# Performance work log

Hardware: AMD Instinct MI355X
Metric: run time of the kernel (lower is better)

Reference implementation:

```python
import jax, jax.numpy as jnp
import numpy as np

N, E, G = 50000, 600000, 512   # nodes, edges, graphs
F, D, L = 128, 128, 3          # in_features, hidden dim, num_gc_layers
ED = D * L                      # embedding_dim (readout='concat')
C = 1.0                         # curvature
MIN_NORM = 1e-15
BALL_EPS = 4e-3                 # hgcn PoincareBall proj eps for float32


def _logmap0(p, c):
    sc = jnp.sqrt(c)
    n = jnp.clip(jnp.linalg.norm(p, axis=-1, keepdims=True), MIN_NORM, None)
    return p / (sc * n) * jnp.arctanh(jnp.clip(sc * n, -1 + 1e-15, 1 - 1e-15))


def _expmap0(u, c):
    sc = jnp.sqrt(c)
    n = jnp.clip(jnp.linalg.norm(u, axis=-1, keepdims=True), MIN_NORM, None)
    return jnp.tanh(sc * n) * u / (sc * n)


def _proj(x, c):
    n = jnp.clip(jnp.linalg.norm(x, axis=-1, keepdims=True), MIN_NORM, None)
    maxn = (1.0 - BALL_EPS) / jnp.sqrt(c)
    return jnp.where(n > maxn, x / n * maxn, x)


def _gcn(x, W, b, src, dst):
    h = x @ W
    deg = jax.ops.segment_sum(jnp.ones_like(dst, dtype=h.dtype), dst, num_segments=N) + 1.0
    dinv = deg ** -0.5
    msg = h[src] * (dinv[src] * dinv[dst])[:, None]           # [E, D]
    agg = jax.ops.segment_sum(msg, dst, num_segments=N) + h * (dinv * dinv)[:, None]
    return agg + b


def _encoder(x, Ws, bs, src, dst, batch):
    xs = []
    for W, b in zip(Ws, bs):
        x = jax.nn.relu(_gcn(x, W, b, src, dst))
        xs.append(x)
    # readout='concat' with global_add_pool
    g = jnp.concatenate([jax.ops.segment_sum(h, batch, num_segments=G) for h in xs], axis=1)
    return g, jnp.concatenate(xs, axis=1)


def _mlp(x, W1, W2):  # proj_head: Linear (no bias), ReLU, Linear (no bias)
    return jax.nn.relu(x @ W1) @ W2


def setup_inputs() -> dict:
    key = jax.random.key(0)
    ks = jax.random.split(key, 24)

    def xav(k, i, o):
        return jax.random.normal(k, (i, o), dtype=jnp.float32) * np.float32(np.sqrt(2.0 / (i + o)))

    inp = {
        'x':   jax.random.normal(ks[0], (N, F), dtype=jnp.float32) * 1e-3,  # points inside the ball
        'x_s': jax.random.normal(ks[1], (N, F), dtype=jnp.float32) * 1e-3,
        'src': jax.random.randint(ks[2], (E,), 0, N, dtype=jnp.int32),
        'dst': jax.random.randint(ks[3], (E,), 0, N, dtype=jnp.int32),
        'batch': jnp.sort(jax.random.randint(ks[4], (N,), 0, G, dtype=jnp.int32)),
        # feature-branch GCN encoder
        'Wf0': xav(ks[5], F, D), 'Wf1': xav(ks[6], D, D), 'Wf2': xav(ks[7], D, D),
        'bf0': jnp.zeros((D,), jnp.float32), 'bf1': jnp.zeros((D,), jnp.float32), 'bf2': jnp.zeros((D,), jnp.float32),
        # structure-branch GCN encoder
        'Ws0': xav(ks[8], F, D), 'Ws1': xav(ks[9], D, D), 'Ws2': xav(ks[10], D, D),
        'bs0': jnp.zeros((D,), jnp.float32), 'bs1': jnp.zeros((D,), jnp.float32), 'bs2': jnp.zeros((D,), jnp.float32),
        # proj heads (biases removed by init_emb)
        'P1': xav(ks[11], ED, ED), 'P2': xav(ks[12], ED, ED),
        'G1': xav(ks[13], 2 * ED, ED), 'G2': xav(ks[14], ED, ED),
    }
    return inp


def reference(x, x_s, Wf0, Wf1, Wf2, bf0, bf1, bf2, Ws0, Ws1, Ws2, bs0, bs1, bs2, P1, P2, G1, G2, src, dst, batch):
    xt_f = _logmap0(x, C)
    xt_s = _logmap0(x_s, C)
    g_f, n_f = _encoder(xt_f, (Wf0, Wf1, Wf2), (bf0, bf1, bf2), src, dst, batch)
    g_s, n_s = _encoder(xt_s, (Ws0, Ws1, Ws2), (bs0, bs1, bs2), src, dst, batch)
    g = _mlp(jnp.concatenate((g_f, g_s), axis=1), G1, G2)
    e = lambda t: _proj(_expmap0(t, C), C)
    return (e(g), e(_mlp(g_f, P1, P2)), e(_mlp(n_f, P1, P2)), e(_mlp(g_s, P1, P2)), e(_mlp(n_s, P1, P2)))
```

## Files before the change

### kernel.cpp

```cpp
#include <hip/hip_runtime.h>
#include <math.h>

#define N_NODES 50000
#define N_EDGES 600000
#define N_GRAPHS 512
#define F_IN 128
#define D_HID 128
#define EDIM 384
#define M_ALL (N_NODES + N_GRAPHS)

typedef __attribute__((ext_vector_type(8))) short bf16x8;
typedef __attribute__((ext_vector_type(4))) float f32x4;

static __device__ __forceinline__ float wave_reduce_sum(float s) {
#pragma unroll
  for (int off = 32; off > 0; off >>= 1) s += __shfl_xor(s, off, 64);
  return s;
}

static __device__ __forceinline__ int wave_reduce_sum_i(int s) {
#pragma unroll
  for (int off = 32; off > 0; off >>= 1) s += __shfl_xor(s, off, 64);
  return s;
}

static __device__ __forceinline__ short f2b(float f) {
  unsigned u = __float_as_uint(f);
  unsigned r = (u + 0x7FFFu + ((u >> 16) & 1u)) >> 16;
  return (short)r;
}

static __device__ __forceinline__ float b2f(short s) {
  return __uint_as_float(((unsigned)(unsigned short)s) << 16);
}


#define SCAN_BS 256
#define SCAN_NB ((N_NODES + SCAN_BS - 1) / SCAN_BS)

__global__ __launch_bounds__(SCAN_BS) void init_kernel(const int* __restrict__ batch,
                                                       int* __restrict__ cnt,
                                                       int* __restrict__ gptr) {
  int i = blockIdx.x * SCAN_BS + threadIdx.x;
  if (i < N_NODES) cnt[i] = 0;
  if (i <= N_GRAPHS) {
    int lo = 0, hi = N_NODES;
    while (lo < hi) { int mid = (lo + hi) >> 1; if (batch[mid] < i) lo = mid + 1; else hi = mid; }
    gptr[i] = lo;
  }
}

__global__ void hist_kernel(const int* __restrict__ dst, int* __restrict__ cnt) {
  int i = blockIdx.x * blockDim.x + threadIdx.x;
  if (i < N_EDGES) atomicAdd(&cnt[dst[i]], 1);
}

__global__ __launch_bounds__(SCAN_BS) void scan1_kernel(const int* __restrict__ cnt,
                                                        int* __restrict__ row_ptr,
                                                        int* __restrict__ bsum) {
  __shared__ int wsum[4];
  int tid = threadIdx.x, lane = tid & 63, wid = tid >> 6;
  int idx = blockIdx.x * SCAN_BS + tid;
  int v = (idx < N_NODES) ? cnt[idx] : 0;
  int x = v;
#pragma unroll
  for (int off = 1; off < 64; off <<= 1) {
    int t = __shfl_up(x, off, 64);
    if (lane >= off) x += t;
  }
  if (lane == 63) wsum[wid] = x;
  __syncthreads();
  int pre = 0, tot = 0;
#pragma unroll
  for (int w = 0; w < 4; ++w) { int s = wsum[w]; tot += s; if (w < wid) pre += s; }
  if (idx < N_NODES) row_ptr[idx + 1] = x + pre;
  if (tid == 0) bsum[blockIdx.x] = tot;
}

__global__ __launch_bounds__(SCAN_BS) void scan3_kernel(const int* __restrict__ cnt,
                                                        const int* __restrict__ bsum,
                                                        int* __restrict__ row_ptr,
                                                        int* __restrict__ cursor,
                                                        float* __restrict__ dinv) {
  __shared__ int ws[4];
  int tid = threadIdx.x, lane = tid & 63, wid = tid >> 6;
  int v = 0;
  if (tid < SCAN_NB && tid < blockIdx.x) v = bsum[tid];
  v = wave_reduce_sum_i(v);
  if (lane == 0) ws[wid] = v;
  __syncthreads();
  int boff = ws[0] + ws[1] + ws[2] + ws[3];
  int idx = blockIdx.x * SCAN_BS + tid;
  if (idx >= N_NODES) return;
  int val = row_ptr[idx + 1] + boff;
  row_ptr[idx + 1] = val;
  int c = cnt[idx];
  cursor[idx] = val - c;
  dinv[idx] = 1.0f / sqrtf((float)(c + 1));
  if (idx == 0) row_ptr[0] = 0;
}

__global__ void scatter_kernel(const int* __restrict__ src, const int* __restrict__ dst,
                               const float* __restrict__ dinv, int* __restrict__ cursor,
                               int* __restrict__ col, float* __restrict__ ew) {
  int e = blockIdx.x * blockDim.x + threadIdx.x;
  if (e >= N_EDGES) return;
  int s = src[e], d = dst[e];
  int pos = atomicAdd(&cursor[d], 1);
  col[pos] = s;
  ew[pos] = dinv[s] * dinv[d];
}


struct WcSeg { const float* W; short* Wt; int K; int Nc; };
struct WcArgs { WcSeg seg[10]; };

__global__ void wconv_all_kernel(WcArgs a) {
  int sidx = blockIdx.y;
  WcSeg s = a.seg[sidx];
  int i = blockIdx.x * blockDim.x + threadIdx.x;
  if (i >= s.K * s.Nc) return;
  int k = i / s.Nc, n = i - k * s.Nc;
  s.Wt[(size_t)n * s.K + k] = f2b(s.W[i]);
}


__global__ __launch_bounds__(256) void logmap2_kernel(const float* __restrict__ x,
                                                      const float* __restrict__ x_s,
                                                      short* __restrict__ Ab) {
  int w = blockIdx.x * 4 + (threadIdx.x >> 6);
  int lane = threadIdx.x & 63;
  if (w >= 2 * N_NODES) return;
  int br = (w >= N_NODES) ? 1 : 0;
  int row = br ? (w - N_NODES) : w;
  const float* xr = (br ? x_s : x) + (size_t)row * F_IN;
  float2 v = *(const float2*)(xr + lane * 2);
  float s = wave_reduce_sum(v.x * v.x + v.y * v.y);
  float n = sqrtf(s);
  float nc = fmaxf(n, 1e-15f);
  float f = atanhf(fminf(nc, 0.9999999f)) / nc;
  short2 o; o.x = f2b(v.x * f); o.y = f2b(v.y * f);
  *(short2*)(Ab + (size_t)row * 256 + br * 128 + lane * 2) = o;
}


__global__ __launch_bounds__(256) void agg2_kernel(const short* __restrict__ Xin, int lda,
                                                   const float* __restrict__ dinv,
                                                   const int* __restrict__ row_ptr,
                                                   const int* __restrict__ col,
                                                   const float* __restrict__ ew,
                                                   short* __restrict__ Xa) {
  int node = blockIdx.x * 4 + (threadIdx.x >> 6);
  int lane = threadIdx.x & 63;
  if (node >= N_NODES) return;
  float di = dinv[node];
  float wsf = di * di;
  short4 sv = *(const short4*)(Xin + (size_t)node * lda + lane * 4);
  float a0 = b2f(sv.x) * wsf, a1 = b2f(sv.y) * wsf, a2 = b2f(sv.z) * wsf, a3 = b2f(sv.w) * wsf;
  int s = row_ptr[node], e = row_ptr[node + 1];
  int j = s;
  for (; j + 4 <= e; j += 4) {
    int c0 = col[j], c1 = col[j + 1], c2 = col[j + 2], c3 = col[j + 3];
    float w0 = ew[j], w1 = ew[j + 1], w2 = ew[j + 2], w3 = ew[j + 3];
    short4 v0 = *(const short4*)(Xin + (size_t)c0 * lda + lane * 4);
    short4 v1 = *(const short4*)(Xin + (size_t)c1 * lda + lane * 4);
    short4 v2 = *(const short4*)(Xin + (size_t)c2 * lda + lane * 4);
    short4 v3 = *(const short4*)(Xin + (size_t)c3 * lda + lane * 4);
    a0 += b2f(v0.x) * w0; a1 += b2f(v0.y) * w0; a2 += b2f(v0.z) * w0; a3 += b2f(v0.w) * w0;
    a0 += b2f(v1.x) * w1; a1 += b2f(v1.y) * w1; a2 += b2f(v1.z) * w1; a3 += b2f(v1.w) * w1;
    a0 += b2f(v2.x) * w2; a1 += b2f(v2.y) * w2; a2 += b2f(v2.z) * w2; a3 += b2f(v2.w) * w2;
    a0 += b2f(v3.x) * w3; a1 += b2f(v3.y) * w3; a2 += b2f(v3.z) * w3; a3 += b2f(v3.w) * w3;
  }
  for (; j < e; ++j) {
    float w0 = ew[j];
    short4 v0 = *(const short4*)(Xin + (size_t)col[j] * lda + lane * 4);
    a0 += b2f(v0.x) * w0; a1 += b2f(v0.y) * w0; a2 += b2f(v0.z) * w0; a3 += b2f(v0.w) * w0;
  }
  short4 o; o.x = f2b(a0); o.y = f2b(a1); o.z = f2b(a2); o.w = f2b(a3);
  *(short4*)(Xa + (size_t)node * 256 + lane * 4) = o;
}


#define LDK 40

struct GemmZArgs {
  const short* A[2];
  const short* Bt[2];
  const float* bias[2];
  short* Cb[2];
  int lda, ldc, M, Nc, K, kexp, do_relu;
};

__global__ __launch_bounds__(256) void mfma_gemmz_kernel(GemmZArgs g) {
  __shared__ __align__(16) short As[128 * LDK];
  __shared__ __align__(16) short Bs[128 * LDK];
  int z = blockIdx.z;
  const short* __restrict__ A = g.A[z];
  const short* __restrict__ Bt = g.Bt[z];
  int tid = threadIdx.x;
  int wave = tid >> 6, lane = tid & 63;
  int wr = (wave >> 1) * 64, wc = (wave & 1) * 64;
  int q = lane >> 4, m = lane & 15;
  int row0 = blockIdx.x * 128, col0 = blockIdx.y * 128;
  f32x4 acc[4][4] = {};
  for (int k0 = 0; k0 < g.K; k0 += 32) {
#pragma unroll
    for (int p = 0; p < 2; ++p) {
      int idx = p * 256 + tid;
      int r = idx >> 2, kc = (idx & 3) * 8;
      int gr = row0 + r;
      int kk = k0 + kc;
      int acol = g.kexp ? (kk + ((kk >> 7) << 7)) : kk;
      float4 v = make_float4(0.f, 0.f, 0.f, 0.f);
      if (gr < g.M) v = *(const float4*)(A + (size_t)gr * g.lda + acol);
      *(float4*)(As + r * LDK + kc) = v;
      float4 w = *(const float4*)(Bt + (size_t)(col0 + r) * g.K + kk);
      *(float4*)(Bs + r * LDK + kc) = w;
    }
    __syncthreads();
    bf16x8 af[4], bfr[4];
#pragma unroll
    for (int i = 0; i < 4; ++i) {
      af[i]  = *(const bf16x8*)(As + (wr + i * 16 + m) * LDK + q * 8);
      bfr[i] = *(const bf16x8*)(Bs + (wc + i * 16 + m) * LDK + q * 8);
    }
#pragma unroll
    for (int i = 0; i < 4; ++i)
#pragma unroll
      for (int j = 0; j < 4; ++j)
        acc[i][j] = __builtin_amdgcn_mfma_f32_16x16x32_bf16(af[i], bfr[j], acc[i][j], 0, 0, 0);
    __syncthreads();
  }
  const float* __restrict__ bias = g.bias[z];
  short* __restrict__ Cb = g.Cb[z];
#pragma unroll
  for (int i = 0; i < 4; ++i) {
#pragma unroll
    for (int r = 0; r < 4; ++r) {
      int rr = row0 + wr + i * 16 + q * 4 + r;
      if (rr >= g.M) continue;
#pragma unroll
      for (int j = 0; j < 4; ++j) {
        int cc = col0 + wc + j * 16 + m;
        float v = acc[i][j][r];
        if (bias) v += bias[cc];
        if (g.do_relu) v = fmaxf(v, 0.0f);
        Cb[(size_t)rr * g.ldc + cc] = f2b(v);
      }
    }
  }
}


struct Head2Args {
  const short* A[2];
  const short* Bt2;
  float* Cf[2];
  float* Cf2[2];
  int lda, M, split;
};

__global__ __launch_bounds__(512) void head2_kernel(Head2Args g) {
  __shared__ __align__(16) short As[128 * LDK];
  __shared__ __align__(16) short Bs[384 * LDK];
  int z = blockIdx.z;
  const short* __restrict__ A = g.A[z];
  const short* __restrict__ Bt = g.Bt2;
  int tid = threadIdx.x;
  int wave = tid >> 6, lane = tid & 63;
  int q = lane >> 4, m = lane & 15;
  int row0 = blockIdx.x * 128;
  f32x4 acc[24] = {};
  for (int k0 = 0; k0 < 384; k0 += 32) {
    {
      int r = tid >> 2, kc = (tid & 3) * 8;
      int gr = row0 + r;
      float4 v = make_float4(0.f, 0.f, 0.f, 0.f);
      if (gr < g.M) v = *(const float4*)(A + (size_t)gr * g.lda + k0 + kc);
      *(float4*)(As + r * LDK + kc) = v;
    }
#pragma unroll
    for (int p = 0; p < 3; ++p) {
      int idx = p * 512 + tid;
      int r = idx >> 2, kc = (idx & 3) * 8;
      float4 w0 = *(const float4*)(Bt + (size_t)r * 384 + k0 + kc);
      *(float4*)(Bs + r * LDK + kc) = w0;
    }
    __syncthreads();
    bf16x8 af = *(const bf16x8*)(As + (wave * 16 + m) * LDK + q * 8);
#pragma unroll
    for (int j = 0; j < 24; ++j) {
      bf16x8 bfr = *(const bf16x8*)(Bs + (j * 16 + m) * LDK + q * 8);
      acc[j] = __builtin_amdgcn_mfma_f32_16x16x32_bf16(af, bfr, acc[j], 0, 0, 0);
    }
    __syncthreads();
  }
  float* __restrict__ Cf = g.Cf[z];
  float* __restrict__ Cf2 = g.Cf2[z];
  const float maxn = 1.0f - 4e-3f;
#pragma unroll
  for (int r = 0; r < 4; ++r) {
    float s = 0.0f;
#pragma unroll
    for (int j = 0; j < 24; ++j) s += acc[j][r] * acc[j][r];
    s += __shfl_xor(s, 1, 64);
    s += __shfl_xor(s, 2, 64);
    s += __shfl_xor(s, 4, 64);
    s += __shfl_xor(s, 8, 64);
    int rr = row0 + wave * 16 + q * 4 + r;
    if (rr >= g.M) continue;
    float n = fmaxf(sqrtf(s), 1e-15f);
    float th = tanhf(n);
    float f = th / n;
    float n2 = fmaxf(th, 1e-15f);
    if (n2 > maxn) f *= maxn / n2;
    if (rr < g.split) {
#pragma unroll
      for (int j = 0; j < 24; ++j) Cf[(size_t)rr * 384 + j * 16 + m] = acc[j][r] * f;
    } else {
#pragma unroll
      for (int j = 0; j < 24; ++j) Cf2[(size_t)(rr - g.split) * 384 + j * 16 + m] = acc[j][r] * f;
    }
  }
}


__global__ __launch_bounds__(768) void pool2_kernel(const short* __restrict__ NB,
                                                    const int* __restrict__ gptr,
                                                    short* __restrict__ GCb,
                                                    short* __restrict__ nbappend) {
  int g = blockIdx.x, t = threadIdx.x;
  int s = gptr[g], e = gptr[g + 1];
  float acc = 0.0f;
  for (int i = s; i < e; ++i) acc += b2f(NB[(size_t)i * 768 + t]);
  short bv = f2b(acc);
  int l = t >> 8, rem = t & 255, b = rem >> 7, c = rem & 127;
  GCb[(size_t)g * 768 + b * 384 + l * 128 + c] = bv;
  nbappend[(size_t)g * 768 + t] = bv;
}


extern "C" void kernel_launch(void* const* d_in, const int* in_sizes, int n_in,
                              void* d_out, int out_size, void* d_ws, size_t ws_size,
                              hipStream_t stream) {
  (void)in_sizes; (void)n_in; (void)out_size; (void)ws_size;
  const float* x   = (const float*)d_in[0];
  const float* x_s = (const float*)d_in[1];
  const int* src   = (const int*)d_in[2];
  const int* dst   = (const int*)d_in[3];
  const int* batch = (const int*)d_in[4];
  const float* Wf[3] = {(const float*)d_in[5], (const float*)d_in[6], (const float*)d_in[7]};
  const float* bf[3] = {(const float*)d_in[8], (const float*)d_in[9], (const float*)d_in[10]};
  const float* Wsb[3] = {(const float*)d_in[11], (const float*)d_in[12], (const float*)d_in[13]};
  const float* bs[3] = {(const float*)d_in[14], (const float*)d_in[15], (const float*)d_in[16]};
  const float* P1 = (const float*)d_in[17];
  const float* P2 = (const float*)d_in[18];
  const float* G1 = (const float*)d_in[19];
  const float* G2 = (const float*)d_in[20];
  float* out = (float*)d_out;

  char* w = (char*)d_ws;
  auto alloc = [&](size_t bytes) {
    char* p = w;
    w += (bytes + 255) & ~(size_t)255;
    return p;
  };
  short* HIDb2 = (short*)alloc((size_t)2 * M_ALL * 384 * 2);
  short* Ab    = HIDb2;
  short* Xa    = (short*)alloc((size_t)N_NODES * 256 * 2);
  short* NB    = (short*)alloc((size_t)M_ALL * 768 * 2);
  int* cnt     = (int*)alloc((size_t)N_NODES * 4);
  int* row_ptr = (int*)alloc((size_t)(N_NODES + 1) * 4);
  int* cursor  = (int*)alloc((size_t)N_NODES * 4);
  float* dinv  = (float*)alloc((size_t)N_NODES * 4);
  int* col     = (int*)alloc((size_t)N_EDGES * 4);
  float* ew    = (float*)alloc((size_t)N_EDGES * 4);
  int* gptr    = (int*)alloc((size_t)(N_GRAPHS + 1) * 4);
  int* bsum    = (int*)alloc(256 * 4);
  short* GCb   = (short*)alloc((size_t)N_GRAPHS * 768 * 2);
  short* GHb   = (short*)alloc((size_t)N_GRAPHS * 384 * 2);
  short* P1t   = (short*)alloc((size_t)EDIM * EDIM * 2);
  short* P2t   = (short*)alloc((size_t)EDIM * EDIM * 2);
  short* G1t   = (short*)alloc((size_t)768 * EDIM * 2);
  short* G2t   = (short*)alloc((size_t)EDIM * EDIM * 2);
  short* Wft[3], *Wst[3];
  for (int l = 0; l < 3; ++l) {
    Wft[l] = (short*)alloc((size_t)128 * 128 * 2);
    Wst[l] = (short*)alloc((size_t)128 * 128 * 2);
  }

  {
    WcArgs wa;
    wa.seg[0] = {P1, P1t, EDIM, EDIM};
    wa.seg[1] = {P2, P2t, EDIM, EDIM};
    wa.seg[2] = {G1, G1t, 768, EDIM};
    wa.seg[3] = {G2, G2t, EDIM, EDIM};
    for (int l = 0; l < 3; ++l) {
      wa.seg[4 + l] = {Wf[l], Wft[l], 128, 128};
      wa.seg[7 + l] = {Wsb[l], Wst[l], 128, 128};
    }
    wconv_all_kernel<<<dim3((768 * EDIM + 255) / 256, 10), 256, 0, stream>>>(wa);
  }

  init_kernel<<<SCAN_NB, SCAN_BS, 0, stream>>>(batch, cnt, gptr);
  hist_kernel<<<(N_EDGES + 255) / 256, 256, 0, stream>>>(dst, cnt);
  scan1_kernel<<<SCAN_NB, SCAN_BS, 0, stream>>>(cnt, row_ptr, bsum);
  scan3_kernel<<<SCAN_NB, SCAN_BS, 0, stream>>>(cnt, bsum, row_ptr, cursor, dinv);
  scatter_kernel<<<(N_EDGES + 255) / 256, 256, 0, stream>>>(src, dst, dinv, cursor, col, ew);

  const size_t OUT0 = 0;
  const size_t OUT1 = (size_t)N_GRAPHS * EDIM;
  const size_t OUT2 = OUT1 + (size_t)N_GRAPHS * EDIM;
  const size_t OUT3 = OUT2 + (size_t)N_NODES * EDIM;

  const int gx_layer = (N_NODES + 127) / 128;
  const int gx_mfma  = (M_ALL + 127) / 128;
  const int gx_agg   = (N_NODES + 3) / 4;

  logmap2_kernel<<<(2 * N_NODES + 3) / 4, 256, 0, stream>>>(x, x_s, Ab);

  const short* cur = Ab;
  int clda = 256;
  for (int l = 0; l < 3; ++l) {
    agg2_kernel<<<gx_agg, 256, 0, stream>>>(cur, clda, dinv, row_ptr, col, ew, Xa);
    GemmZArgs ga = {};
    ga.A[0] = Xa;        ga.A[1] = Xa + 128;
    ga.Bt[0] = Wft[l];   ga.Bt[1] = Wst[l];
    ga.bias[0] = bf[l];  ga.bias[1] = bs[l];
    ga.Cb[0] = NB + l * 256;        ga.Cb[1] = NB + l * 256 + 128;
    ga.lda = 256; ga.ldc = 768; ga.M = N_NODES; ga.Nc = 128; ga.K = 128;
    ga.kexp = 0; ga.do_relu = 1;
    mfma_gemmz_kernel<<<dim3(gx_layer, 1, 2), 256, 0, stream>>>(ga);
    cur = NB + l * 256;
    clda = 768;
  }

  pool2_kernel<<<N_GRAPHS, 768, 0, stream>>>(NB, gptr, GCb, NB + (size_t)N_NODES * 768);

  const int gx_g = (N_GRAPHS + 127) / 128;
  {
    GemmZArgs g1 = {};
    g1.A[0] = g1.A[1] = GCb;
    g1.Bt[0] = g1.Bt[1] = G1t;
    g1.Cb[0] = g1.Cb[1] = GHb;
    g1.lda = 768; g1.ldc = 384; g1.M = N_GRAPHS; g1.Nc = EDIM; g1.K = 768;
    g1.kexp = 0; g1.do_relu = 1;
    mfma_gemmz_kernel<<<dim3(gx_g, 3, 1), 256, 0, stream>>>(g1);

    Head2Args g2 = {};
    g2.A[0] = g2.A[1] = GHb;
    g2.Bt2 = G2t;
    g2.Cf[0] = g2.Cf[1] = out + OUT0;
    g2.Cf2[0] = g2.Cf2[1] = out + OUT0;
    g2.lda = 384; g2.M = N_GRAPHS; g2.split = 1 << 30;
    head2_kernel<<<dim3(gx_g, 1, 1), 512, 0, stream>>>(g2);
  }

  float* ghead_out[2] = {out + OUT1, out + OUT3};
  float* node_out[2]  = {out + OUT2, out + OUT3 + (size_t)N_GRAPHS * EDIM};
  {
    GemmZArgs h1 = {};
    h1.A[0] = NB;                 h1.A[1] = NB + 128;
    h1.Bt[0] = h1.Bt[1] = P1t;
    h1.Cb[0] = HIDb2;             h1.Cb[1] = HIDb2 + (size_t)M_ALL * 384;
    h1.lda = 768; h1.ldc = 384; h1.M = M_ALL; h1.Nc = EDIM; h1.K = EDIM;
    h1.kexp = 1; h1.do_relu = 1;
    mfma_gemmz_kernel<<<dim3(gx_mfma, 3, 2), 256, 0, stream>>>(h1);

    Head2Args h2 = {};
    h2.A[0] = HIDb2;              h2.A[1] = HIDb2 + (size_t)M_ALL * 384;
    h2.Bt2 = P2t;
    h2.Cf[0] = node_out[0];       h2.Cf[1] = node_out[1];
    h2.Cf2[0] = ghead_out[0];     h2.Cf2[1] = ghead_out[1];
    h2.lda = 384; h2.M = M_ALL; h2.split = N_NODES;
    head2_kernel<<<dim3(gx_mfma, 1, 2), 512, 0, stream>>>(h2);
  }
}
```

Baseline: 770.5 us.

## Fuse both projection-head MLP layers into one kernel keeping hidden in LDS

```diff
diff --git a/kernel.cpp b/kernel.cpp
--- a/kernel.cpp
+++ b/kernel.cpp
@@ -252,74 +252,130 @@
 }
 
 
-struct Head2Args {
+#define HLD 392
+
+struct Mlp2Args {
   const short* A[2];
-  const short* Bt2;
+  const short* B1;
+  const short* B2;
   float* Cf[2];
   float* Cf2[2];
-  int lda, M, split;
+  int lda, M, K1, kexp, split;
 };
 
-__global__ __launch_bounds__(512) void head2_kernel(Head2Args g) {
+__global__ __launch_bounds__(512, 2) void mlp2_kernel(Mlp2Args g) {
   __shared__ __align__(16) short As[128 * LDK];
   __shared__ __align__(16) short Bs[384 * LDK];
+  __shared__ __align__(16) short H[128 * HLD];
+  __shared__ float nsum[128][2];
   int z = blockIdx.z;
   const short* __restrict__ A = g.A[z];
-  const short* __restrict__ Bt = g.Bt2;
   int tid = threadIdx.x;
   int wave = tid >> 6, lane = tid & 63;
   int q = lane >> 4, m = lane & 15;
+  int rbase = (wave & 3) * 32;
+  int cg = wave >> 2;
   int row0 = blockIdx.x * 128;
-  f32x4 acc[24] = {};
-  for (int k0 = 0; k0 < 384; k0 += 32) {
+  f32x4 acc[2][12] = {};
+  for (int k0 = 0; k0 < g.K1; k0 += 32) {
     {
       int r = tid >> 2, kc = (tid & 3) * 8;
       int gr = row0 + r;
+      int kk = k0 + kc;
+      int acol = g.kexp ? (kk + ((kk >> 7) << 7)) : kk;
       float4 v = make_float4(0.f, 0.f, 0.f, 0.f);
-      if (gr < g.M) v = *(const float4*)(A + (size_t)gr * g.lda + k0 + kc);
+      if (gr < g.M) v = *(const float4*)(A + (size_t)gr * g.lda + acol);
       *(float4*)(As + r * LDK + kc) = v;
     }
 #pragma unroll
     for (int p = 0; p < 3; ++p) {
       int idx = p * 512 + tid;
       int r = idx >> 2, kc = (idx & 3) * 8;
-      float4 w0 = *(const float4*)(Bt + (size_t)r * 384 + k0 + kc);
+      float4 w0 = *(const float4*)(g.B1 + (size_t)r * g.K1 + k0 + kc);
       *(float4*)(Bs + r * LDK + kc) = w0;
     }
     __syncthreads();
-    bf16x8 af = *(const bf16x8*)(As + (wave * 16 + m) * LDK + q * 8);
-#pragma unroll
-    for (int j = 0; j < 24; ++j) {
-      bf16x8 bfr = *(const bf16x8*)(Bs + (j * 16 + m) * LDK + q * 8);
-      acc[j] = __builtin_amdgcn_mfma_f32_16x16x32_bf16(af, bfr, acc[j], 0, 0, 0);
+    bf16x8 af0 = *(const bf16x8*)(As + (rbase + m) * LDK + q * 8);
+    bf16x8 af1 = *(const bf16x8*)(As + (rbase + 16 + m) * LDK + q * 8);
+#pragma unroll
+    for (int j = 0; j < 12; ++j) {
+      bf16x8 bfr = *(const bf16x8*)(Bs + (cg * 192 + j * 16 + m) * LDK + q * 8);
+      acc[0][j] = __builtin_amdgcn_mfma_f32_16x16x32_bf16(af0, bfr, acc[0][j], 0, 0, 0);
+      acc[1][j] = __builtin_amdgcn_mfma_f32_16x16x32_bf16(af1, bfr, acc[1][j], 0, 0, 0);
     }
     __syncthreads();
   }
+#pragma unroll
+  for (int sub = 0; sub < 2; ++sub)
+#pragma unroll
+    for (int j = 0; j < 12; ++j)
+#pragma unroll
+      for (int r = 0; r < 4; ++r)
+        H[(rbase + sub * 16 + q * 4 + r) * HLD + cg * 192 + j * 16 + m] =
+            f2b(fmaxf(acc[sub][j][r], 0.0f));
+#pragma unroll
+  for (int sub = 0; sub < 2; ++sub)
+#pragma unroll
+    for (int j = 0; j < 12; ++j) acc[sub][j] = (f32x4){0.f, 0.f, 0.f, 0.f};
+  for (int k0 = 0; k0 < 384; k0 += 32) {
+#pragma unroll
+    for (int p = 0; p < 3; ++p) {
+      int idx = p * 512 + tid;
+      int r = idx >> 2, kc = (idx & 3) * 8;
+      float4 w0 = *(const float4*)(g.B2 + (size_t)r * 384 + k0 + kc);
+      *(float4*)(Bs + r * LDK + kc) = w0;
+    }
+    __syncthreads();
+    bf16x8 af0 = *(const bf16x8*)(H + (rbase + m) * HLD + k0 + q * 8);
+    bf16x8 af1 = *(const bf16x8*)(H + (rbase + 16 + m) * HLD + k0 + q * 8);
+#pragma unroll
+    for (int j = 0; j < 12; ++j) {
+      bf16x8 bfr = *(const bf16x8*)(Bs + (cg * 192 + j * 16 + m) * LDK + q * 8);
+      acc[0][j] = __builtin_amdgcn_mfma_f32_16x16x32_bf16(af0, bfr, acc[0][j], 0, 0, 0);
+      acc[1][j] = __builtin_amdgcn_mfma_f32_16x16x32_bf16(af1, bfr, acc[1][j], 0, 0, 0);
+    }
+    __syncthreads();
+  }
+#pragma unroll
+  for (int sub = 0; sub < 2; ++sub) {
+#pragma unroll
+    for (int r = 0; r < 4; ++r) {
+      float s = 0.0f;
+#pragma unroll
+      for (int j = 0; j < 12; ++j) s += acc[sub][j][r] * acc[sub][j][r];
+      s += __shfl_xor(s, 1, 64);
+      s += __shfl_xor(s, 2, 64);
+      s += __shfl_xor(s, 4, 64);
+      s += __shfl_xor(s, 8, 64);
+      if (m == 0) nsum[rbase + sub * 16 + q * 4 + r][cg] = s;
+    }
+  }
+  __syncthreads();
+  const float maxn = 1.0f - 4e-3f;
   float* __restrict__ Cf = g.Cf[z];
   float* __restrict__ Cf2 = g.Cf2[z];
-  const float maxn = 1.0f - 4e-3f;
-#pragma unroll
-  for (int r = 0; r < 4; ++r) {
-    float s = 0.0f;
-#pragma unroll
-    for (int j = 0; j < 24; ++j) s += acc[j][r] * acc[j][r];
-    s += __shfl_xor(s, 1, 64);
-    s += __shfl_xor(s, 2, 64);
-    s += __shfl_xor(s, 4, 64);
-    s += __shfl_xor(s, 8, 64);
-    int rr = row0 + wave * 16 + q * 4 + r;
-    if (rr >= g.M) continue;
-    float n = fmaxf(sqrtf(s), 1e-15f);
-    float th = tanhf(n);
-    float f = th / n;
-    float n2 = fmaxf(th, 1e-15f);
-    if (n2 > maxn) f *= maxn / n2;
-    if (rr < g.split) {
-#pragma unroll
-      for (int j = 0; j < 24; ++j) Cf[(size_t)rr * 384 + j * 16 + m] = acc[j][r] * f;
-    } else {
-#pragma unroll
-      for (int j = 0; j < 24; ++j) Cf2[(size_t)(rr - g.split) * 384 + j * 16 + m] = acc[j][r] * f;
+#pragma unroll
+  for (int sub = 0; sub < 2; ++sub) {
+#pragma unroll
+    for (int r = 0; r < 4; ++r) {
+      int rl = rbase + sub * 16 + q * 4 + r;
+      int rr = row0 + rl;
+      if (rr >= g.M) continue;
+      float s = nsum[rl][0] + nsum[rl][1];
+      float n = fmaxf(sqrtf(s), 1e-15f);
+      float th = tanhf(n);
+      float f = th / n;
+      float n2 = fmaxf(th, 1e-15f);
+      if (n2 > maxn) f *= maxn / n2;
+      if (rr < g.split) {
+#pragma unroll
+        for (int j = 0; j < 12; ++j)
+          Cf[(size_t)rr * 384 + cg * 192 + j * 16 + m] = acc[sub][j][r] * f;
+      } else {
+#pragma unroll
+        for (int j = 0; j < 12; ++j)
+          Cf2[(size_t)(rr - g.split) * 384 + cg * 192 + j * 16 + m] = acc[sub][j][r] * f;
+      }
     }
   }
 }
@@ -365,8 +421,7 @@
     w += (bytes + 255) & ~(size_t)255;
     return p;
   };
-  short* HIDb2 = (short*)alloc((size_t)2 * M_ALL * 384 * 2);
-  short* Ab    = HIDb2;
+  short* Ab    = (short*)alloc((size_t)N_NODES * 256 * 2);
   short* Xa    = (short*)alloc((size_t)N_NODES * 256 * 2);
   short* NB    = (short*)alloc((size_t)M_ALL * 768 * 2);
   int* cnt     = (int*)alloc((size_t)N_NODES * 4);
@@ -378,7 +433,6 @@
   int* gptr    = (int*)alloc((size_t)(N_GRAPHS + 1) * 4);
   int* bsum    = (int*)alloc(256 * 4);
   short* GCb   = (short*)alloc((size_t)N_GRAPHS * 768 * 2);
-  short* GHb   = (short*)alloc((size_t)N_GRAPHS * 384 * 2);
   short* P1t   = (short*)alloc((size_t)EDIM * EDIM * 2);
   short* P2t   = (short*)alloc((size_t)EDIM * EDIM * 2);
   short* G1t   = (short*)alloc((size_t)768 * EDIM * 2);
@@ -437,42 +491,23 @@
 
   pool2_kernel<<<N_GRAPHS, 768, 0, stream>>>(NB, gptr, GCb, NB + (size_t)N_NODES * 768);
 
-  const int gx_g = (N_GRAPHS + 127) / 128;
   {
-    GemmZArgs g1 = {};
-    g1.A[0] = g1.A[1] = GCb;
-    g1.Bt[0] = g1.Bt[1] = G1t;
-    g1.Cb[0] = g1.Cb[1] = GHb;
-    g1.lda = 768; g1.ldc = 384; g1.M = N_GRAPHS; g1.Nc = EDIM; g1.K = 768;
-    g1.kexp = 0; g1.do_relu = 1;
-    mfma_gemmz_kernel<<<dim3(gx_g, 3, 1), 256, 0, stream>>>(g1);
-
-    Head2Args g2 = {};
-    g2.A[0] = g2.A[1] = GHb;
-    g2.Bt2 = G2t;
-    g2.Cf[0] = g2.Cf[1] = out + OUT0;
-    g2.Cf2[0] = g2.Cf2[1] = out + OUT0;
-    g2.lda = 384; g2.M = N_GRAPHS; g2.split = 1 << 30;
-    head2_kernel<<<dim3(gx_g, 1, 1), 512, 0, stream>>>(g2);
-  }
-
-  float* ghead_out[2] = {out + OUT1, out + OUT3};
-  float* node_out[2]  = {out + OUT2, out + OUT3 + (size_t)N_GRAPHS * EDIM};
+    Mlp2Args gh = {};
+    gh.A[0] = gh.A[1] = GCb;
+    gh.B1 = G1t; gh.B2 = G2t;
+    gh.Cf[0] = gh.Cf[1] = out + OUT0;
+    gh.Cf2[0] = gh.Cf2[1] = out + OUT0;
+    gh.lda = 768; gh.M = N_GRAPHS; gh.K1 = 768; gh.kexp = 0; gh.split = 1 << 30;
+    mlp2_kernel<<<dim3((N_GRAPHS + 127) / 128, 1, 1), 512, 0, stream>>>(gh);
+  }
+
   {
-    GemmZArgs h1 = {};
-    h1.A[0] = NB;                 h1.A[1] = NB + 128;
-    h1.Bt[0] = h1.Bt[1] = P1t;
-    h1.Cb[0] = HIDb2;             h1.Cb[1] = HIDb2 + (size_t)M_ALL * 384;
-    h1.lda = 768; h1.ldc = 384; h1.M = M_ALL; h1.Nc = EDIM; h1.K = EDIM;
-    h1.kexp = 1; h1.do_relu = 1;
-    mfma_gemmz_kernel<<<dim3(gx_mfma, 3, 2), 256, 0, stream>>>(h1);
-
-    Head2Args h2 = {};
-    h2.A[0] = HIDb2;              h2.A[1] = HIDb2 + (size_t)M_ALL * 384;
-    h2.Bt2 = P2t;
-    h2.Cf[0] = node_out[0];       h2.Cf[1] = node_out[1];
-    h2.Cf2[0] = ghead_out[0];     h2.Cf2[1] = ghead_out[1];
-    h2.lda = 384; h2.M = M_ALL; h2.split = N_NODES;
-    head2_kernel<<<dim3(gx_mfma, 1, 2), 512, 0, stream>>>(h2);
-  }
-}
+    Mlp2Args h = {};
+    h.A[0] = NB;                  h.A[1] = NB + 128;
+    h.B1 = P1t; h.B2 = P2t;
+    h.Cf[0] = out + OUT2;         h.Cf[1] = out + OUT3 + (size_t)N_GRAPHS * EDIM;
+    h.Cf2[0] = out + OUT1;        h.Cf2[1] = out + OUT3;
+    h.lda = 768; h.M = M_ALL; h.K1 = EDIM; h.kexp = 1; h.split = N_NODES;
+    mlp2_kernel<<<dim3(gx_mfma, 1, 2), 512, 0, stream>>>(h);
+  }
+}
```

After: 766.6 us. About the same (-0.5%).

## Fuse two-layer projection MLPs into one kernel with hidden activations in LDS

Applied to the files above, without the earlier changes.

```diff
diff --git a/kernel.cpp b/kernel.cpp
--- a/kernel.cpp
+++ b/kernel.cpp
@@ -11,6 +11,7 @@
 
 typedef __attribute__((ext_vector_type(8))) short bf16x8;
 typedef __attribute__((ext_vector_type(4))) float f32x4;
+typedef __attribute__((ext_vector_type(16))) float f32x16;
 
 static __device__ __forceinline__ float wave_reduce_sum(float s) {
 #pragma unroll
@@ -252,76 +253,123 @@
 }
 
 
-struct Head2Args {
-  const short* A[2];
-  const short* Bt2;
-  float* Cf[2];
-  float* Cf2[2];
-  int lda, M, split;
+#define HLD 392
+
+struct MlpProb {
+  const short* A;
+  const short* B1;
+  const short* B2;
+  float* Cf;
+  float* Cf2;
+  int lda, M, K1, kexp, split;
 };
-
-__global__ __launch_bounds__(512) void head2_kernel(Head2Args g) {
-  __shared__ __align__(16) short As[128 * LDK];
-  __shared__ __align__(16) short Bs[384 * LDK];
+struct Mlp2Args { MlpProb p[3]; int gx_h; };
+
+__global__ __launch_bounds__(512) void mlp2_kernel(Mlp2Args g) {
+  __shared__ __align__(16) short H[128 * HLD];
+  __shared__ float nsum[128][4];
   int z = blockIdx.z;
-  const short* __restrict__ A = g.A[z];
-  const short* __restrict__ Bt = g.Bt2;
+  int bx = blockIdx.x;
+  MlpProb p;
+  int row0;
+  if (bx < g.gx_h) { p = g.p[z]; row0 = bx * 128; }
+  else { if (z) return; p = g.p[2]; row0 = (bx - g.gx_h) * 128; }
+
   int tid = threadIdx.x;
   int wave = tid >> 6, lane = tid & 63;
-  int q = lane >> 4, m = lane & 15;
-  int row0 = blockIdx.x * 128;
-  f32x4 acc[24] = {};
-  for (int k0 = 0; k0 < 384; k0 += 32) {
-    {
-      int r = tid >> 2, kc = (tid & 3) * 8;
-      int gr = row0 + r;
-      float4 v = make_float4(0.f, 0.f, 0.f, 0.f);
-      if (gr < g.M) v = *(const float4*)(A + (size_t)gr * g.lda + k0 + kc);
-      *(float4*)(As + r * LDK + kc) = v;
-    }
-#pragma unroll
-    for (int p = 0; p < 3; ++p) {
-      int idx = p * 512 + tid;
-      int r = idx >> 2, kc = (idx & 3) * 8;
-      float4 w0 = *(const float4*)(Bt + (size_t)r * 384 + k0 + kc);
-      *(float4*)(Bs + r * LDK + kc) = w0;
-    }
-    __syncthreads();
-    bf16x8 af = *(const bf16x8*)(As + (wave * 16 + m) * LDK + q * 8);
-#pragma unroll
-    for (int j = 0; j < 24; ++j) {
-      bf16x8 bfr = *(const bf16x8*)(Bs + (j * 16 + m) * LDK + q * 8);
-      acc[j] = __builtin_amdgcn_mfma_f32_16x16x32_bf16(af, bfr, acc[j], 0, 0, 0);
-    }
-    __syncthreads();
-  }
-  float* __restrict__ Cf = g.Cf[z];
-  float* __restrict__ Cf2 = g.Cf2[z];
+  int l31 = lane & 31, lh = lane >> 5;
+  int rg = wave & 1;
+  int cq = wave >> 1;
+
+  const short* Arow0 = p.A + (size_t)(row0 + rg * 64 + l31) * p.lda;
+  const short* Arow1 = Arow0 + (size_t)32 * p.lda;
+  const short* B1c0 = p.B1 + (size_t)(cq * 96 + l31) * p.K1;
+  const short* B1c1 = B1c0 + (size_t)32 * p.K1;
+  const short* B1c2 = B1c1 + (size_t)32 * p.K1;
+
+  f32x16 acc0[2][3] = {};
+#pragma unroll 2
+  for (int k0 = 0; k0 < p.K1; k0 += 16) {
+    int kk = k0 + lh * 8;
+    int acol = p.kexp ? (kk + ((kk >> 7) << 7)) : kk;
+    bf16x8 a0 = *(const bf16x8*)(Arow0 + acol);
+    bf16x8 a1 = *(const bf16x8*)(Arow1 + acol);
+    bf16x8 b0 = *(const bf16x8*)(B1c0 + kk);
+    bf16x8 b1 = *(const bf16x8*)(B1c1 + kk);
+    bf16x8 b2 = *(const bf16x8*)(B1c2 + kk);
+    acc0[0][0] = __builtin_amdgcn_mfma_f32_32x32x16_bf16(a0, b0, acc0[0][0], 0, 0, 0);
+    acc0[1][0] = __builtin_amdgcn_mfma_f32_32x32x16_bf16(a1, b0, acc0[1][0], 0, 0, 0);
+    acc0[0][1] = __builtin_amdgcn_mfma_f32_32x32x16_bf16(a0, b1, acc0[0][1], 0, 0, 0);
+    acc0[1][1] = __builtin_amdgcn_mfma_f32_32x32x16_bf16(a1, b1, acc0[1][1], 0, 0, 0);
+    acc0[0][2] = __builtin_amdgcn_mfma_f32_32x32x16_bf16(a0, b2, acc0[0][2], 0, 0, 0);
+    acc0[1][2] = __builtin_amdgcn_mfma_f32_32x32x16_bf16(a1, b2, acc0[1][2], 0, 0, 0);
+  }
+#pragma unroll
+  for (int rf = 0; rf < 2; ++rf)
+#pragma unroll
+    for (int f = 0; f < 3; ++f)
+#pragma unroll
+      for (int reg = 0; reg < 16; ++reg) {
+        int rl = rg * 64 + rf * 32 + (reg & 3) + 8 * (reg >> 2) + 4 * lh;
+        H[rl * HLD + cq * 96 + f * 32 + l31] = f2b(fmaxf(acc0[rf][f][reg], 0.0f));
+      }
+  __syncthreads();
+  const short* B2c0 = p.B2 + (size_t)(cq * 96 + l31) * 384;
+  const short* B2c1 = B2c0 + (size_t)32 * 384;
+  const short* B2c2 = B2c1 + (size_t)32 * 384;
+  const short* H0 = H + (rg * 64 + l31) * HLD;
+  const short* H1 = H0 + 32 * HLD;
+  f32x16 acc[2][3] = {};
+#pragma unroll 2
+  for (int k0 = 0; k0 < 384; k0 += 16) {
+    int kk = k0 + lh * 8;
+    bf16x8 a0 = *(const bf16x8*)(H0 + kk);
+    bf16x8 a1 = *(const bf16x8*)(H1 + kk);
+    bf16x8 b0 = *(const bf16x8*)(B2c0 + kk);
+    bf16x8 b1 = *(const bf16x8*)(B2c1 + kk);
+    bf16x8 b2 = *(const bf16x8*)(B2c2 + kk);
+    acc[0][0] = __builtin_amdgcn_mfma_f32_32x32x16_bf16(a0, b0, acc[0][0], 0, 0, 0);
+    acc[1][0] = __builtin_amdgcn_mfma_f32_32x32x16_bf16(a1, b0, acc[1][0], 0, 0, 0);
+    acc[0][1] = __builtin_amdgcn_mfma_f32_32x32x16_bf16(a0, b1, acc[0][1], 0, 0, 0);
+    acc[1][1] = __builtin_amdgcn_mfma_f32_32x32x16_bf16(a1, b1, acc[1][1], 0, 0, 0);
+    acc[0][2] = __builtin_amdgcn_mfma_f32_32x32x16_bf16(a0, b2, acc[0][2], 0, 0, 0);
+    acc[1][2] = __builtin_amdgcn_mfma_f32_32x32x16_bf16(a1, b2, acc[1][2], 0, 0, 0);
+  }
+#pragma unroll
+  for (int rf = 0; rf < 2; ++rf)
+#pragma unroll
+    for (int reg = 0; reg < 16; ++reg) {
+      float s = acc[rf][0][reg] * acc[rf][0][reg] + acc[rf][1][reg] * acc[rf][1][reg] +
+                acc[rf][2][reg] * acc[rf][2][reg];
+      s += __shfl_xor(s, 1, 64);
+      s += __shfl_xor(s, 2, 64);
+      s += __shfl_xor(s, 4, 64);
+      s += __shfl_xor(s, 8, 64);
+      s += __shfl_xor(s, 16, 64);
+      if (l31 == 0)
+        nsum[rg * 64 + rf * 32 + (reg & 3) + 8 * (reg >> 2) + 4 * lh][cq] = s;
+    }
+  __syncthreads();
   const float maxn = 1.0f - 4e-3f;
 #pragma unroll
-  for (int r = 0; r < 4; ++r) {
-    float s = 0.0f;
-#pragma unroll
-    for (int j = 0; j < 24; ++j) s += acc[j][r] * acc[j][r];
-    s += __shfl_xor(s, 1, 64);
-    s += __shfl_xor(s, 2, 64);
-    s += __shfl_xor(s, 4, 64);
-    s += __shfl_xor(s, 8, 64);
-    int rr = row0 + wave * 16 + q * 4 + r;
-    if (rr >= g.M) continue;
-    float n = fmaxf(sqrtf(s), 1e-15f);
-    float th = tanhf(n);
-    float f = th / n;
-    float n2 = fmaxf(th, 1e-15f);
-    if (n2 > maxn) f *= maxn / n2;
-    if (rr < g.split) {
-#pragma unroll
-      for (int j = 0; j < 24; ++j) Cf[(size_t)rr * 384 + j * 16 + m] = acc[j][r] * f;
-    } else {
-#pragma unroll
-      for (int j = 0; j < 24; ++j) Cf2[(size_t)(rr - g.split) * 384 + j * 16 + m] = acc[j][r] * f;
-    }
-  }
+  for (int rf = 0; rf < 2; ++rf)
+#pragma unroll
+    for (int reg = 0; reg < 16; ++reg) {
+      int rl = rg * 64 + rf * 32 + (reg & 3) + 8 * (reg >> 2) + 4 * lh;
+      int rr = row0 + rl;
+      if (rr >= p.M) continue;
+      float s = nsum[rl][0] + nsum[rl][1] + nsum[rl][2] + nsum[rl][3];
+      float n = fmaxf(sqrtf(s), 1e-15f);
+      float th = tanhf(n);
+      float fct = th / n;
+      float n2 = fmaxf(th, 1e-15f);
+      if (n2 > maxn) fct *= maxn / n2;
+      float* base = (rr < p.split) ? (p.Cf + (size_t)rr * 384)
+                                   : (p.Cf2 + (size_t)(rr - p.split) * 384);
+#pragma unroll
+      for (int f = 0; f < 3; ++f)
+        base[cq * 96 + f * 32 + l31] = acc[rf][f][reg] * fct;
+    }
 }
 
 
@@ -365,8 +413,7 @@
     w += (bytes + 255) & ~(size_t)255;
     return p;
   };
-  short* HIDb2 = (short*)alloc((size_t)2 * M_ALL * 384 * 2);
-  short* Ab    = HIDb2;
+  short* Ab    = (short*)alloc((size_t)N_NODES * 256 * 2);
   short* Xa    = (short*)alloc((size_t)N_NODES * 256 * 2);
   short* NB    = (short*)alloc((size_t)M_ALL * 768 * 2);
   int* cnt     = (int*)alloc((size_t)N_NODES * 4);
@@ -378,7 +425,6 @@
   int* gptr    = (int*)alloc((size_t)(N_GRAPHS + 1) * 4);
   int* bsum    = (int*)alloc(256 * 4);
   short* GCb   = (short*)alloc((size_t)N_GRAPHS * 768 * 2);
-  short* GHb   = (short*)alloc((size_t)N_GRAPHS * 384 * 2);
   short* P1t   = (short*)alloc((size_t)EDIM * EDIM * 2);
   short* P2t   = (short*)alloc((size_t)EDIM * EDIM * 2);
   short* G1t   = (short*)alloc((size_t)768 * EDIM * 2);
@@ -437,42 +483,15 @@
 
   pool2_kernel<<<N_GRAPHS, 768, 0, stream>>>(NB, gptr, GCb, NB + (size_t)N_NODES * 768);
 
-  const int gx_g = (N_GRAPHS + 127) / 128;
   {
-    GemmZArgs g1 = {};
-    g1.A[0] = g1.A[1] = GCb;
-    g1.Bt[0] = g1.Bt[1] = G1t;
-    g1.Cb[0] = g1.Cb[1] = GHb;
-    g1.lda = 768; g1.ldc = 384; g1.M = N_GRAPHS; g1.Nc = EDIM; g1.K = 768;
-    g1.kexp = 0; g1.do_relu = 1;
-    mfma_gemmz_kernel<<<dim3(gx_g, 3, 1), 256, 0, stream>>>(g1);
-
-    Head2Args g2 = {};
-    g2.A[0] = g2.A[1] = GHb;
-    g2.Bt2 = G2t;
-    g2.Cf[0] = g2.Cf[1] = out + OUT0;
-    g2.Cf2[0] = g2.Cf2[1] = out + OUT0;
-    g2.lda = 384; g2.M = N_GRAPHS; g2.split = 1 << 30;
-    head2_kernel<<<dim3(gx_g, 1, 1), 512, 0, stream>>>(g2);
-  }
-
-  float* ghead_out[2] = {out + OUT1, out + OUT3};
-  float* node_out[2]  = {out + OUT2, out + OUT3 + (size_t)N_GRAPHS * EDIM};
-  {
-    GemmZArgs h1 = {};
-    h1.A[0] = NB;                 h1.A[1] = NB + 128;
-    h1.Bt[0] = h1.Bt[1] = P1t;
-    h1.Cb[0] = HIDb2;             h1.Cb[1] = HIDb2 + (size_t)M_ALL * 384;
-    h1.lda = 768; h1.ldc = 384; h1.M = M_ALL; h1.Nc = EDIM; h1.K = EDIM;
-    h1.kexp = 1; h1.do_relu = 1;
-    mfma_gemmz_kernel<<<dim3(gx_mfma, 3, 2), 256, 0, stream>>>(h1);
-
-    Head2Args h2 = {};
-    h2.A[0] = HIDb2;              h2.A[1] = HIDb2 + (size_t)M_ALL * 384;
-    h2.Bt2 = P2t;
-    h2.Cf[0] = node_out[0];       h2.Cf[1] = node_out[1];
-    h2.Cf2[0] = ghead_out[0];     h2.Cf2[1] = ghead_out[1];
-    h2.lda = 384; h2.M = M_ALL; h2.split = N_NODES;
-    head2_kernel<<<dim3(gx_mfma, 1, 2), 512, 0, stream>>>(h2);
-  }
-}
+    const int gx_g = (N_GRAPHS + 127) / 128;
+    Mlp2Args h = {};
+    h.p[0] = {NB,       P1t, P2t, out + OUT2,
+              out + OUT1, 768, M_ALL, EDIM, 1, N_NODES};
+    h.p[1] = {NB + 128, P1t, P2t, out + OUT3 + (size_t)N_GRAPHS * EDIM,
+              out + OUT3, 768, M_ALL, EDIM, 1, N_NODES};
+    h.p[2] = {GCb, G1t, G2t, out + OUT0, out + OUT0, 768, N_GRAPHS, 768, 0, 1 << 30};
+    h.gx_h = gx_mfma;
+    mlp2_kernel<<<dim3(gx_mfma + gx_g, 1, 2), 512, 0, stream>>>(h);
+  }
+}
```

New measurement: 835.6 us. +8.5%, slower.
